# Kernel tuning notes

Hardware: AMD Instinct MI355X
Metric: run time of the kernel (lower is better)

## Reference

```python
import jax, jax.numpy as jnp
import numpy as np

D_IN = 1024
D_OUT = 1024


def setup_inputs() -> dict:
    key = jax.random.key(0)
    k_x, k_q, k_k, k_v = jax.random.split(key, 4)
    x = jax.random.normal(k_x, (8, 2048, D_IN), dtype=jnp.float32)
    s = 1.0 / np.sqrt(D_IN)
    W_query = jax.random.uniform(k_q, (D_IN, D_OUT), jnp.float32, -s, s)
    W_key = jax.random.uniform(k_k, (D_IN, D_OUT), jnp.float32, -s, s)
    W_value = jax.random.uniform(k_v, (D_IN, D_OUT), jnp.float32, -s, s)
    return {"x": x, "W_query": W_query, "W_key": W_key, "W_value": W_value}


def reference(x, W_query, W_key, W_value):
    # x: [B, N, d_in]; weights stored as [d_in, d_out] (already transposed vs torch Linear)
    B, N, _ = x.shape
    q = x @ W_query          # [B, N, d_out]
    k = x @ W_key
    v = x @ W_value
    scores = jnp.einsum('bnd,bmd->bnm', q, k)  # [B, N, N]
    causal = jnp.tril(jnp.ones((N, N), dtype=bool))
    scores = jnp.where(causal, scores, -jnp.inf)
    weights = jax.nn.softmax(scores / np.sqrt(D_OUT), axis=-1)
    # dropout p=0.0 -> identity
    return jnp.einsum('bnm,bmd->bnd', weights, v)
```

## Files before the change

### kernel.cpp

```cpp
#include <hip/hip_runtime.h>
#include <hip/hip_bf16.h>

typedef unsigned short u16;
typedef unsigned int u32;
typedef __bf16 bf16x8 __attribute__((ext_vector_type(8)));
typedef float f32x4 __attribute__((ext_vector_type(4)));
typedef unsigned int u32x4 __attribute__((ext_vector_type(4)));

#define BATCH 8
#define SEQ   2048
#define DIM   1024
#define M_TOT (BATCH * SEQ)
#define N_QKV (3 * DIM)

#define OFF_QKV  ((size_t)0)
#define OFF_VT   ((size_t)100663296)
#define OFF_C    ((size_t)134217728)
#define OFF_XB   OFF_C
#define OFF_WT   (OFF_C + (size_t)33554432)
#define OFF_S    OFF_C

__device__ __forceinline__ u16 f32_to_bf16(float f) {
    u32 u = __builtin_bit_cast(u32, f);
    u = (u + 0x7fffu + ((u >> 16) & 1u)) >> 16;
    return (u16)u;
}

__device__ __forceinline__ float bf16_to_f32(u16 h) {
    u32 u = ((u32)h) << 16;
    return __builtin_bit_cast(float, u);
}

__device__ __forceinline__ bf16x8 lds_load8(const u16* p) {
    return __builtin_bit_cast(bf16x8, *(const u32x4*)p);
}

#define UNIT 8192

__device__ __forceinline__ void stage_unit(const u16* g, size_t lda, int k0,
                                           u16* lds, int tid) {
    int wv = tid >> 6;
#pragma unroll
    for (int iss = 0; iss < 2; ++iss) {
        int s = iss * 512 + tid;
        int o = s & 31;
        int p = o >> 3;
        int q = o & 7;
        int row = ((s >> 5) << 3) + (p << 1) + (q & 1);
        int kg = ((q - (p << 1) - (q & 1)) & 7) >> 1;
        const u16* gp = g + (size_t)row * lda + (k0 + (kg << 3));
        u16* lp = lds + (size_t)(iss * 512 + wv * 64) * 8;
        __builtin_amdgcn_global_load_lds((const __attribute__((address_space(1))) void*)gp,
                                         (__attribute__((address_space(3))) void*)lp,
                                         16, 0, 0);
    }
}

template <int MH>
__device__ __forceinline__ void mfma_phase(const u16* uA, const u16* uB, int lane,
                                           int wm, int wn, f32x4 acc[8][4]) {
    int lrow = lane & 15;
    int kgl = lane >> 4;
    int rb = lrow >> 3;
    int base_l = ((lrow >> 1) & 3) * 64 + ((lrow + 2 * kgl) & 7) * 8;
    bf16x8 a[4], b[4];
#pragma unroll
    for (int i = 0; i < 4; ++i) {
        a[i] = lds_load8(&uA[(size_t)((wm * 16 + (MH * 4 + i) * 2 + rb) * 256 + base_l)]);
        b[i] = lds_load8(&uB[(size_t)((wn * 8 + i * 2 + rb) * 256 + base_l)]);
    }
    __builtin_amdgcn_s_setprio(1);
#pragma unroll
    for (int i = 0; i < 4; ++i)
#pragma unroll
        for (int j = 0; j < 4; ++j)
            acc[MH * 4 + i][j] =
                __builtin_amdgcn_mfma_f32_16x16x32_bf16(a[i], b[j], acc[MH * 4 + i][j], 0, 0, 0);
    __builtin_amdgcn_s_setprio(0);
}

__device__ __forceinline__ void gemm_block_256(const u16* __restrict__ A, size_t lda,
                                               const u16* __restrict__ B, size_t ldb,
                                               int KT, u16* lds, int tid,
                                               f32x4 acc[8][4]) {
    int lane = tid & 63;
    int wv = tid >> 6;
    int wm = wv >> 2, wn = wv & 3;
    stage_unit(A, lda, 0,  lds + 0 * UNIT, tid);
    stage_unit(B, ldb, 0,  lds + 4 * UNIT, tid);
    stage_unit(A, lda, 32, lds + 1 * UNIT, tid);
    stage_unit(B, ldb, 32, lds + 5 * UNIT, tid);
    for (int t = 0; t < KT; ++t) {
        int p = t & 1, pn = p ^ 1;
        int kb = (t + 1) << 6;
        bool pf = (t + 1 < KT);
        asm volatile("s_waitcnt vmcnt(4)" ::: "memory");
        __builtin_amdgcn_s_barrier();
        if (pf) stage_unit(A, lda, kb, lds + (size_t)(pn * 2) * UNIT, tid);
        mfma_phase<0>(lds + (size_t)(p * 2) * UNIT, lds + (size_t)(4 + p * 2) * UNIT,
                      lane, wm, wn, acc);
        __builtin_amdgcn_s_barrier();
        if (pf) stage_unit(B, ldb, kb, lds + (size_t)(4 + pn * 2) * UNIT, tid);
        mfma_phase<1>(lds + (size_t)(p * 2) * UNIT, lds + (size_t)(4 + p * 2) * UNIT,
                      lane, wm, wn, acc);
        __builtin_amdgcn_s_barrier();
        if (pf) { asm volatile("s_waitcnt vmcnt(4)" ::: "memory"); }
        else    { asm volatile("s_waitcnt vmcnt(0)" ::: "memory"); }
        __builtin_amdgcn_s_barrier();
        if (pf) stage_unit(A, lda, kb + 32, lds + (size_t)(pn * 2 + 1) * UNIT, tid);
        mfma_phase<0>(lds + (size_t)(p * 2 + 1) * UNIT, lds + (size_t)(4 + p * 2 + 1) * UNIT,
                      lane, wm, wn, acc);
        __builtin_amdgcn_s_barrier();
        if (pf) stage_unit(B, ldb, kb + 32, lds + (size_t)(4 + pn * 2 + 1) * UNIT, tid);
        mfma_phase<1>(lds + (size_t)(p * 2 + 1) * UNIT, lds + (size_t)(4 + p * 2 + 1) * UNIT,
                      lane, wm, wn, acc);
    }
}

__global__ __launch_bounds__(256) void cast_x_kernel(const float* __restrict__ x,
                                                     u16* __restrict__ xb) {
    size_t g = (size_t)blockIdx.x * 256 + threadIdx.x;
    f32x4 v = ((const f32x4*)x)[g];
    u16 o[4] = {f32_to_bf16(v.x), f32_to_bf16(v.y), f32_to_bf16(v.z), f32_to_bf16(v.w)};
    *(unsigned long long*)(xb + g * 4) = *(const unsigned long long*)o;
}

__global__ __launch_bounds__(256) void transpose_w_kernel(const float* __restrict__ wq,
                                                          const float* __restrict__ wk,
                                                          const float* __restrict__ wv,
                                                          u16* __restrict__ wt) {
    __shared__ __align__(16) u16 tile[64][80];
    const float* w = blockIdx.z == 0 ? wq : (blockIdx.z == 1 ? wk : wv);
    int k0 = blockIdx.x * 64, n0 = blockIdx.y * 64;
    for (int g = threadIdx.x; g < 1024; g += 256) {
        int r = g >> 4, c = (g & 15) << 2;
        f32x4 v = *(const f32x4*)(w + (size_t)(k0 + r) * 1024 + n0 + c);
        tile[r][c + 0] = f32_to_bf16(v.x);
        tile[r][c + 1] = f32_to_bf16(v.y);
        tile[r][c + 2] = f32_to_bf16(v.z);
        tile[r][c + 3] = f32_to_bf16(v.w);
    }
    __syncthreads();
    u16* out = wt + (size_t)blockIdx.z * 1024 * 1024;
    for (int g = threadIdx.x; g < 512; g += 256) {
        int nr = g >> 3, kc = (g & 7) << 3;
        __align__(16) u16 tmp[8];
#pragma unroll
        for (int i = 0; i < 8; ++i) tmp[i] = tile[kc + i][nr];
        *(u32x4*)(out + (size_t)(n0 + nr) * 1024 + k0 + kc) = *(const u32x4*)tmp;
    }
}

__global__ __launch_bounds__(512, 2) void gemm_qkv_kernel(const u16* __restrict__ xb,
                                                          const u16* __restrict__ wt,
                                                          u16* __restrict__ qkv) {
    __shared__ __align__(16) u16 lds[8 * UNIT];
    int wg = blockIdx.x;
    int qx = gridDim.x >> 3;
    int swz = (wg & 7) * qx + (wg >> 3);
    int mt = swz / 12, nt = swz - mt * 12;
    const u16* A = xb + (size_t)mt * 256 * 1024;
    const u16* B = wt + (size_t)nt * 256 * 1024;
    int tid = threadIdx.x;
    f32x4 acc[8][4] = {};
    gemm_block_256(A, 1024, B, 1024, 16, lds, tid, acc);
    int lane = tid & 63, wv = tid >> 6;
    int wm = wv >> 2, wn = wv & 3;
    int r0 = (lane >> 4) << 2, c0 = lane & 15;
    size_t mbase = (size_t)mt * 256 + wm * 128;
    int nbase = nt * 256 + wn * 64;
#pragma unroll
    for (int i = 0; i < 8; ++i)
#pragma unroll
        for (int j = 0; j < 4; ++j) {
            int col = nbase + j * 16 + c0;
            float scale = (col < 1024) ? 0.03125f : 1.0f;
#pragma unroll
            for (int r = 0; r < 4; ++r) {
                size_t row = mbase + i * 16 + r0 + r;
                qkv[row * (size_t)N_QKV + col] = f32_to_bf16(acc[i][j][r] * scale);
            }
        }
}

__global__ __launch_bounds__(256) void transpose_v_kernel(const u16* __restrict__ qkv,
                                                          u16* __restrict__ vt) {
    __shared__ __align__(16) u16 tile[64][80];
    int m0 = blockIdx.x * 64, d0 = blockIdx.y * 64, b = blockIdx.z;
    const u16* src = qkv + (size_t)b * SEQ * N_QKV + 2048;
    for (int g = threadIdx.x; g < 512; g += 256) {
        int r = g >> 3, c = (g & 7) << 3;
        *(u32x4*)&tile[r][c] = *(const u32x4*)(src + (size_t)(m0 + r) * N_QKV + d0 + c);
    }
    __syncthreads();
    u16* dst = vt + (size_t)b * DIM * SEQ;
    for (int g = threadIdx.x; g < 512; g += 256) {
        int dr = g >> 3, mc = (g & 7) << 3;
        __align__(16) u16 tmp[8];
#pragma unroll
        for (int i = 0; i < 8; ++i) tmp[i] = tile[mc + i][dr];
        *(u32x4*)(dst + (size_t)(d0 + dr) * SEQ + m0 + mc) = *(const u32x4*)tmp;
    }
}

__global__ __launch_bounds__(512, 2) void gemm_scores_kernel(const u16* __restrict__ qkv,
                                                             u16* __restrict__ S) {
    __shared__ __align__(16) u16 lds[8 * UNIT];
    int t = blockIdx.x;
    int b = blockIdx.y;
    int ntile = 0;
#pragma unroll
    for (int it = 1; it < 8; ++it)
        if ((it * (it + 1)) / 2 <= t) ntile = it;
    int mtile = t - (ntile * (ntile + 1)) / 2;
    const u16* A = qkv + (size_t)b * SEQ * N_QKV + (size_t)ntile * 256 * N_QKV;
    const u16* B = qkv + (size_t)b * SEQ * N_QKV + (size_t)mtile * 256 * N_QKV + 1024;
    int tid = threadIdx.x;
    f32x4 acc[8][4] = {};
    gemm_block_256(A, N_QKV, B, N_QKV, 16, lds, tid, acc);
    u16* out = S + (size_t)b * SEQ * SEQ + (size_t)ntile * 256 * SEQ + (size_t)mtile * 256;
    int lane = tid & 63, wv = tid >> 6;
    int wm = wv >> 2, wn = wv & 3;
    int r0 = (lane >> 4) << 2, c0 = lane & 15;
#pragma unroll
    for (int i = 0; i < 8; ++i)
#pragma unroll
        for (int j = 0; j < 4; ++j) {
            int col = wn * 64 + j * 16 + c0;
#pragma unroll
            for (int r = 0; r < 4; ++r) {
                int row = wm * 128 + i * 16 + r0 + r;
                out[(size_t)row * SEQ + col] = f32_to_bf16(acc[i][j][r]);
            }
        }
}

__global__ __launch_bounds__(256) void softmax_kernel(u16* __restrict__ SP) {
    int gr = blockIdx.x;
    int n = gr & 2047;
    u16* s = SP + (size_t)gr * SEQ;
    __shared__ float red[4];
    int t = threadIdx.x;
    int base = t << 3;
    int len = n + 1;
    float v[8];
    float lmax = -3.0e38f;
    if (base < len) {
        u32x4 raw = *(const u32x4*)(s + base);
        const u16* h = (const u16*)&raw;
#pragma unroll
        for (int i = 0; i < 8; ++i) {
            v[i] = (base + i < len) ? bf16_to_f32(h[i]) : -3.0e38f;
            lmax = fmaxf(lmax, v[i]);
        }
    } else {
#pragma unroll
        for (int i = 0; i < 8; ++i) v[i] = -3.0e38f;
    }
#pragma unroll
    for (int off = 32; off; off >>= 1) lmax = fmaxf(lmax, __shfl_xor(lmax, off, 64));
    if ((t & 63) == 0) red[t >> 6] = lmax;
    __syncthreads();
    float gmax = fmaxf(fmaxf(red[0], red[1]), fmaxf(red[2], red[3]));
    __syncthreads();
    float lsum = 0.f;
#pragma unroll
    for (int i = 0; i < 8; ++i) {
        float e = __expf(v[i] - gmax);
        v[i] = e;
        lsum += e;
    }
#pragma unroll
    for (int off = 32; off; off >>= 1) lsum += __shfl_xor(lsum, off, 64);
    if ((t & 63) == 0) red[t >> 6] = lsum;
    __syncthreads();
    float inv = 1.0f / (red[0] + red[1] + red[2] + red[3]);
    __align__(16) u16 o[8];
#pragma unroll
    for (int i = 0; i < 8; ++i) o[i] = f32_to_bf16(v[i] * inv);
    *(u32x4*)(s + base) = *(const u32x4*)o;
}

__global__ __launch_bounds__(512, 2) void gemm_out_kernel(const u16* __restrict__ P,
                                                          const u16* __restrict__ vt,
                                                          float* __restrict__ O) {
    __shared__ __align__(16) u16 lds[8 * UNIT];
    int dt = blockIdx.x, b = blockIdx.z;
    int ntile = (SEQ / 256 - 1) - blockIdx.y;
    const u16* A = P + (size_t)b * SEQ * SEQ + (size_t)ntile * 256 * SEQ;
    const u16* B = vt + (size_t)b * DIM * SEQ + (size_t)dt * 256 * SEQ;
    int tid = threadIdx.x;
    f32x4 acc[8][4] = {};
    int KT = (ntile + 1) * 4;
    gemm_block_256(A, SEQ, B, SEQ, KT, lds, tid, acc);
    float* out = O + (size_t)b * SEQ * DIM + (size_t)ntile * 256 * DIM + (size_t)dt * 256;
    int lane = tid & 63, wv = tid >> 6;
    int wm = wv >> 2, wn = wv & 3;
    int r0 = (lane >> 4) << 2, c0 = lane & 15;
#pragma unroll
    for (int i = 0; i < 8; ++i)
#pragma unroll
        for (int j = 0; j < 4; ++j) {
            int col = wn * 64 + j * 16 + c0;
#pragma unroll
            for (int r = 0; r < 4; ++r) {
                int row = wm * 128 + i * 16 + r0 + r;
                out[(size_t)row * DIM + col] = acc[i][j][r];
            }
        }
}

extern "C" void kernel_launch(void* const* d_in, const int* in_sizes, int n_in,
                              void* d_out, int out_size, void* d_ws, size_t ws_size,
                              hipStream_t stream) {
    const float* x = (const float*)d_in[0];
    const float* wq = (const float*)d_in[1];
    const float* wk = (const float*)d_in[2];
    const float* wv = (const float*)d_in[3];
    char* ws = (char*)d_ws;
    u16* qkv = (u16*)(ws + OFF_QKV);
    u16* vt = (u16*)(ws + OFF_VT);
    u16* xb = (u16*)(ws + OFF_XB);
    u16* wt = (u16*)(ws + OFF_WT);
    u16* S = (u16*)(ws + OFF_S);
    float* O = (float*)d_out;

    cast_x_kernel<<<M_TOT * DIM / 4 / 256, 256, 0, stream>>>(x, xb);
    transpose_w_kernel<<<dim3(16, 16, 3), 256, 0, stream>>>(wq, wk, wv, wt);
    gemm_qkv_kernel<<<(M_TOT / 256) * (N_QKV / 256), 512, 0, stream>>>(xb, wt, qkv);
    transpose_v_kernel<<<dim3(SEQ / 64, DIM / 64, BATCH), 256, 0, stream>>>(qkv, vt);
    gemm_scores_kernel<<<dim3(36, BATCH), 512, 0, stream>>>(qkv, S);
    softmax_kernel<<<BATCH * SEQ, 256, 0, stream>>>(S);
    gemm_out_kernel<<<dim3(DIM / 256, SEQ / 256, BATCH), 512, 0, stream>>>(S, vt, O);
}
```

Baseline: 386.3 us.

## Restructure GEMM main loop into explicit ds-load / mfma phases with barriers

Splits each MFMA phase into a separate LDS fragment load and compute step. Issues the fragment loads before the next global-to-LDS prefetch, then waits on lgkmcnt and a barrier before the MFMAs, in a ping-pong style schedule. The aim is to overlap LDS reads with global loads and keep the matrix cores fed. It adds more barriers per k-step, and the reordered vmcnt waits could leave correctness fragile if any hazard is missed.

```diff
diff --git a/kernel.cpp b/kernel.cpp
--- a/kernel.cpp
+++ b/kernel.cpp
@@ -57,18 +57,22 @@
 }
 
 template <int MH>
-__device__ __forceinline__ void mfma_phase(const u16* uA, const u16* uB, int lane,
-                                           int wm, int wn, f32x4 acc[8][4]) {
+__device__ __forceinline__ void ds_load_frags(const u16* uA, const u16* uB, int lane,
+                                              int wm, int wn, bf16x8 a[4], bf16x8 b[4]) {
     int lrow = lane & 15;
     int kgl = lane >> 4;
     int rb = lrow >> 3;
     int base_l = ((lrow >> 1) & 3) * 64 + ((lrow + 2 * kgl) & 7) * 8;
-    bf16x8 a[4], b[4];
 #pragma unroll
     for (int i = 0; i < 4; ++i) {
         a[i] = lds_load8(&uA[(size_t)((wm * 16 + (MH * 4 + i) * 2 + rb) * 256 + base_l)]);
         b[i] = lds_load8(&uB[(size_t)((wn * 8 + i * 2 + rb) * 256 + base_l)]);
     }
+}
+
+template <int MH>
+__device__ __forceinline__ void mfma_compute(const bf16x8 a[4], const bf16x8 b[4],
+                                             f32x4 acc[8][4]) {
     __builtin_amdgcn_s_setprio(1);
 #pragma unroll
     for (int i = 0; i < 4; ++i)
@@ -90,30 +94,49 @@
     stage_unit(B, ldb, 0,  lds + 4 * UNIT, tid);
     stage_unit(A, lda, 32, lds + 1 * UNIT, tid);
     stage_unit(B, ldb, 32, lds + 5 * UNIT, tid);
+    asm volatile("s_waitcnt vmcnt(4)" ::: "memory");
+    __builtin_amdgcn_s_barrier();
     for (int t = 0; t < KT; ++t) {
         int p = t & 1, pn = p ^ 1;
         int kb = (t + 1) << 6;
         bool pf = (t + 1 < KT);
-        asm volatile("s_waitcnt vmcnt(4)" ::: "memory");
-        __builtin_amdgcn_s_barrier();
+        const u16* uA0 = lds + (size_t)(p * 2) * UNIT;
+        const u16* uB0 = lds + (size_t)(4 + p * 2) * UNIT;
+        const u16* uA1 = lds + (size_t)(p * 2 + 1) * UNIT;
+        const u16* uB1 = lds + (size_t)(4 + p * 2 + 1) * UNIT;
+        bf16x8 a[4], b[4];
+        ds_load_frags<0>(uA0, uB0, lane, wm, wn, a, b);
         if (pf) stage_unit(A, lda, kb, lds + (size_t)(pn * 2) * UNIT, tid);
-        mfma_phase<0>(lds + (size_t)(p * 2) * UNIT, lds + (size_t)(4 + p * 2) * UNIT,
-                      lane, wm, wn, acc);
-        __builtin_amdgcn_s_barrier();
-        if (pf) stage_unit(B, ldb, kb, lds + (size_t)(4 + pn * 2) * UNIT, tid);
-        mfma_phase<1>(lds + (size_t)(p * 2) * UNIT, lds + (size_t)(4 + p * 2) * UNIT,
-                      lane, wm, wn, acc);
-        __builtin_amdgcn_s_barrier();
-        if (pf) { asm volatile("s_waitcnt vmcnt(4)" ::: "memory"); }
-        else    { asm volatile("s_waitcnt vmcnt(0)" ::: "memory"); }
-        __builtin_amdgcn_s_barrier();
+        __builtin_amdgcn_s_barrier();
+        asm volatile("s_waitcnt lgkmcnt(0)" ::: "memory");
+        mfma_compute<0>(a, b, acc);
+        __builtin_amdgcn_s_barrier();
+        ds_load_frags<1>(uA0, uB0, lane, wm, wn, a, b);
+        if (pf) {
+            stage_unit(B, ldb, kb, lds + (size_t)(4 + pn * 2) * UNIT, tid);
+            asm volatile("s_waitcnt vmcnt(4)" ::: "memory");
+        } else {
+            asm volatile("s_waitcnt vmcnt(0)" ::: "memory");
+        }
+        __builtin_amdgcn_s_barrier();
+        asm volatile("s_waitcnt lgkmcnt(0)" ::: "memory");
+        mfma_compute<1>(a, b, acc);
+        __builtin_amdgcn_s_barrier();
+        ds_load_frags<0>(uA1, uB1, lane, wm, wn, a, b);
         if (pf) stage_unit(A, lda, kb + 32, lds + (size_t)(pn * 2 + 1) * UNIT, tid);
-        mfma_phase<0>(lds + (size_t)(p * 2 + 1) * UNIT, lds + (size_t)(4 + p * 2 + 1) * UNIT,
-                      lane, wm, wn, acc);
-        __builtin_amdgcn_s_barrier();
-        if (pf) stage_unit(B, ldb, kb + 32, lds + (size_t)(4 + pn * 2 + 1) * UNIT, tid);
-        mfma_phase<1>(lds + (size_t)(p * 2 + 1) * UNIT, lds + (size_t)(4 + p * 2 + 1) * UNIT,
-                      lane, wm, wn, acc);
+        __builtin_amdgcn_s_barrier();
+        asm volatile("s_waitcnt lgkmcnt(0)" ::: "memory");
+        mfma_compute<0>(a, b, acc);
+        __builtin_amdgcn_s_barrier();
+        ds_load_frags<1>(uA1, uB1, lane, wm, wn, a, b);
+        if (pf) {
+            stage_unit(B, ldb, kb + 32, lds + (size_t)(4 + pn * 2 + 1) * UNIT, tid);
+            asm volatile("s_waitcnt vmcnt(4)" ::: "memory");
+        }
+        __builtin_amdgcn_s_barrier();
+        asm volatile("s_waitcnt lgkmcnt(0)" ::: "memory");
+        mfma_compute<1>(a, b, acc);
+        __builtin_amdgcn_s_barrier();
     }
 }
 
```

Measured after the change: 400.0 us. +3.5%, slower.
